# Kernel optimization log

Measured on AMD Instinct MI355X. Metric: run time of the kernel, lower is better.

## Reference

```python
import jax, jax.numpy as jnp
import numpy as np

TOP_K = 8


def setup_inputs() -> dict:
    key = jax.random.key(0)
    k1, k2 = jax.random.split(key)
    B, S, D, E = 4, 4096, 2048, 64
    x = jax.random.normal(k1, (B, S, D), dtype=jnp.float32)
    # nn.Linear(d_model, n_experts): weight [E, D], bias [E]
    W = jax.random.normal(k2, (E, D), dtype=jnp.float32) * (1.0 / np.sqrt(D))
    b = jnp.zeros((E,), dtype=jnp.float32)
    return {"x": x, "W": W, "b": b}


def reference(x, W, b):
    # logits: [B, S, E] = x @ W^T + b
    logits = jnp.einsum("bsd,ed->bse", x, W) + b
    scores = jax.nn.sigmoid(logits)                      # [B, S, E]
    B, S, E = scores.shape
    flat = scores.reshape(B * S, E)                      # tokens x experts
    top_w, top_idx = jax.lax.top_k(flat, TOP_K)          # [B*S, k]
    return top_w.reshape(B, S, TOP_K), top_idx.reshape(B, S, TOP_K)
```

## Files before the change

kernel.cpp:

```cpp
#include <hip/hip_runtime.h>
#include <math.h>

#define TOKENS 16384
#define DMODEL 2048
#define NEXP   64
#define TOPK   8
#define BM     32
#define BK     64
#define NCHUNK (DMODEL / BK)
#define ROWU   72
#define WTILEU (NEXP * ROWU)
#define WT3PAD 14336

typedef unsigned short u16;
typedef float f32x4 __attribute__((ext_vector_type(4)));
typedef short s16x8 __attribute__((ext_vector_type(8)));

__device__ __forceinline__ u16 f2bf(float f, float& back) {
    unsigned u = __float_as_uint(f);
    unsigned r = u + 0x7fffu + ((u >> 16) & 1u);
    back = __uint_as_float(r & 0xffff0000u);
    return (u16)(r >> 16);
}

__device__ __forceinline__ void gload_lds16(const void* g, void* l) {
    __builtin_amdgcn_global_load_lds(
        (const __attribute__((address_space(1))) unsigned int*)g,
        (__attribute__((address_space(3))) unsigned int*)l, 16, 0, 0);
}

__global__ __launch_bounds__(256) void wconv(
    const float* __restrict__ W, u16* __restrict__ wimg)
{
    const int id = blockIdx.x * 256 + threadIdx.x;
    const int e = id >> 11;
    const int k = id & 2047;
    const float x = W[id];
    float f1, f2, fd;
    const u16 a = f2bf(x, f1);
    const float d1 = x - f1;
    const u16 b = f2bf(d1, f2);
    const float d2 = d1 - f2;
    const u16 c = f2bf(d2, fd);
    u16* base = wimg + (size_t)(k >> 6) * WT3PAD + e * ROWU + (k & 63);
    base[0]          = a;
    base[WTILEU]     = b;
    base[2 * WTILEU] = c;
}

__global__ __launch_bounds__(256) void router_fused(
    const float* __restrict__ x, const u16* __restrict__ wimg,
    const float* __restrict__ bias, float* __restrict__ out_w,
    float* __restrict__ out_i)
{
    __shared__ __align__(16) u16 xs[3][BM * ROWU];
    __shared__ __align__(16) u16 wsb[2][WT3PAD];
    __shared__ float lg[BM][NEXP + 4];

    const int tid  = threadIdx.x;
    const int lane = tid & 63;
    const int w    = tid >> 6;
    const int wr   = w >> 1;
    const int wc   = w & 1;
    const size_t tokBase = (size_t)blockIdx.x * BM;

    const int srow = tid >> 3;
    const int soct = tid & 7;
    const float* xp = x + (tokBase + srow) * DMODEL + soct * 8;

    const int arow  = wr * 16 + (lane & 15);
    const int kq    = (lane >> 4) * 8;
    const int brow0 = wc * 32 + (lane & 15);

    f32x4  acc[2][2];
    double accd[2][4];
#pragma unroll
    for (int i = 0; i < 2; ++i)
#pragma unroll
        for (int j = 0; j < 2; ++j)
            acc[i][j] = (f32x4){0.f, 0.f, 0.f, 0.f};
#pragma unroll
    for (int j = 0; j < 2; ++j)
#pragma unroll
        for (int r = 0; r < 4; ++r) accd[j][r] = 0.0;

    const char* wgbase = (const char*)wimg;
#define WCOPY(tt, buf)                                                        \
    {                                                                         \
        const char* gsrc_ = wgbase + (size_t)(tt) * (WT3PAD * 2) + w * 1024 + \
                            lane * 16;                                        \
        char* ldst_ = (char*)&wsb[buf][0] + w * 1024;                         \
        _Pragma("unroll") for (int r_ = 0; r_ < 7; ++r_)                      \
            gload_lds16(gsrc_ + r_ * 4096, ldst_ + r_ * 4096);                \
    }

    float4 xa = *(const float4*)(xp);
    float4 xb = *(const float4*)(xp + 4);
    WCOPY(0, 0);

    for (int t = 0; t < NCHUNK; ++t) {
        __syncthreads();
        {
            float xv[8] = {xa.x, xa.y, xa.z, xa.w, xb.x, xb.y, xb.z, xb.w};
            s16x8 va, vb, vc;
#pragma unroll
            for (int j = 0; j < 8; ++j) {
                float f1, f2, fd;
                const u16 a1 = f2bf(xv[j], f1);
                const float d1 = xv[j] - f1;
                const u16 a2 = f2bf(d1, f2);
                const float d2 = d1 - f2;
                const u16 a3 = f2bf(d2, fd);
                va[j] = (short)a1; vb[j] = (short)a2; vc[j] = (short)a3;
            }
            const int ub = srow * ROWU + soct * 8;
            *(s16x8*)&xs[0][ub] = va;
            *(s16x8*)&xs[1][ub] = vb;
            *(s16x8*)&xs[2][ub] = vc;
        }
        __syncthreads();
        if (t + 1 < NCHUNK) {
            xp += BK;
            xa = *(const float4*)(xp);
            xb = *(const float4*)(xp + 4);
            WCOPY(t + 1, (t + 1) & 1);
        }

        const u16* wb = &wsb[t & 1][0];
#pragma unroll
        for (int ks = 0; ks < 2; ++ks) {
            const int ko = ks * 32 + kq;
            const s16x8 a1 = *(const s16x8*)&xs[0][arow * ROWU + ko];
            const s16x8 a2 = *(const s16x8*)&xs[1][arow * ROWU + ko];
            const s16x8 a3 = *(const s16x8*)&xs[2][arow * ROWU + ko];
#pragma unroll
            for (int nt = 0; nt < 2; ++nt) {
                const int br = (brow0 + nt * 16) * ROWU + ko;
                const s16x8 b1 = *(const s16x8*)&wb[0 * WTILEU + br];
                const s16x8 b2 = *(const s16x8*)&wb[1 * WTILEU + br];
                const s16x8 b3 = *(const s16x8*)&wb[2 * WTILEU + br];
                f32x4 t0 = acc[ks][nt];
                t0 = __builtin_amdgcn_mfma_f32_16x16x32_bf16(a1, b1, t0, 0, 0, 0);
                t0 = __builtin_amdgcn_mfma_f32_16x16x32_bf16(a1, b2, t0, 0, 0, 0);
                t0 = __builtin_amdgcn_mfma_f32_16x16x32_bf16(a2, b1, t0, 0, 0, 0);
                t0 = __builtin_amdgcn_mfma_f32_16x16x32_bf16(a1, b3, t0, 0, 0, 0);
                t0 = __builtin_amdgcn_mfma_f32_16x16x32_bf16(a3, b1, t0, 0, 0, 0);
                t0 = __builtin_amdgcn_mfma_f32_16x16x32_bf16(a2, b2, t0, 0, 0, 0);
                acc[ks][nt] = t0;
            }
        }
#pragma unroll
        for (int nt = 0; nt < 2; ++nt)
#pragma unroll
            for (int r = 0; r < 4; ++r) {
                accd[nt][r] += (double)acc[0][nt][r] + (double)acc[1][nt][r];
                acc[0][nt][r] = 0.f;
                acc[1][nt][r] = 0.f;
            }
    }

#pragma unroll
    for (int nt = 0; nt < 2; ++nt)
#pragma unroll
        for (int r = 0; r < 4; ++r) {
            const int row = wr * 16 + (lane >> 4) * 4 + r;
            const int col = wc * 32 + nt * 16 + (lane & 15);
            lg[row][col] = (float)accd[nt][r];
        }
    __syncthreads();

    const float be = bias[lane];
#pragma unroll
    for (int i = 0; i < 8; ++i) {
        const int tl = w * 8 + i;
        float v = lg[tl][lane] + be;
        const int myi = lane;
        float bv = 0.0f; int bi = 0;
#pragma unroll
        for (int r = 0; r < TOPK; ++r) {
            float mv = v; int mi = myi;
#pragma unroll
            for (int off = 32; off > 0; off >>= 1) {
                const float ov = __shfl_xor(mv, off, 64);
                const int   oi = __shfl_xor(mi, off, 64);
                if (ov > mv || (ov == mv && oi < mi)) { mv = ov; mi = oi; }
            }
            if (lane == r) { bv = mv; bi = mi; }
            if (myi == mi) { v = -INFINITY; }
        }
        if (lane < TOPK) {
            const size_t tok = tokBase + tl;
            out_w[tok * TOPK + lane] = 1.0f / (1.0f + expf(-bv));
            out_i[tok * TOPK + lane] = (float)bi;
        }
    }
}

extern "C" void kernel_launch(void* const* d_in, const int* in_sizes, int n_in,
                              void* d_out, int out_size, void* d_ws, size_t ws_size,
                              hipStream_t stream) {
    const float* x    = (const float*)d_in[0];
    const float* W    = (const float*)d_in[1];
    const float* bias = (const float*)d_in[2];
    float* out_w = (float*)d_out;
    float* out_i = (float*)d_out + (size_t)TOKENS * TOPK;
    u16* wimg = (u16*)d_ws;

    wconv<<<dim3((NEXP * DMODEL) / 256), 256, 0, stream>>>(W, wimg);
    router_fused<<<dim3(TOKENS / BM), 256, 0, stream>>>(x, wimg, bias, out_w, out_i);
}
```

Before: 259.4 us.

## Load x fragments directly to registers and pre-swizzle W into MFMA fragment layout

Each thread now loads its own x fragment from global memory straight into registers and splits it into three bf16 parts there, so the x shared-memory staging and one barrier per chunk go away. The weight-prep kernel writes W already arranged in MFMA B-fragment order, so the main kernel reads conflict-free s16x8 values. The weight chunk now goes through registers with a manual double buffer instead of direct global-to-LDS loads. The cost is that each wave repeats the x split for its own tile, register pressure rises, and shared memory is reused for the logits, which lowers the LDS footprint.

```diff
diff --git a/kernel.cpp b/kernel.cpp
--- a/kernel.cpp
+++ b/kernel.cpp
@@ -8,9 +8,8 @@
 #define BM     32
 #define BK     64
 #define NCHUNK (DMODEL / BK)
-#define ROWU   72
-#define WTILEU (NEXP * ROWU)
-#define WT3PAD 14336
+#define WCHUNKB 24576
+#define WSHORTS 12288
 
 typedef unsigned short u16;
 typedef float f32x4 __attribute__((ext_vector_type(4)));
@@ -23,29 +22,38 @@
     return (u16)(r >> 16);
 }
 
-__device__ __forceinline__ void gload_lds16(const void* g, void* l) {
-    __builtin_amdgcn_global_load_lds(
-        (const __attribute__((address_space(1))) unsigned int*)g,
-        (__attribute__((address_space(3))) unsigned int*)l, 16, 0, 0);
-}
-
 __global__ __launch_bounds__(256) void wconv(
     const float* __restrict__ W, u16* __restrict__ wimg)
 {
-    const int id = blockIdx.x * 256 + threadIdx.x;
-    const int e = id >> 11;
-    const int k = id & 2047;
-    const float x = W[id];
-    float f1, f2, fd;
-    const u16 a = f2bf(x, f1);
-    const float d1 = x - f1;
-    const u16 b = f2bf(d1, f2);
-    const float d2 = d1 - f2;
-    const u16 c = f2bf(d2, fd);
-    u16* base = wimg + (size_t)(k >> 6) * WT3PAD + e * ROWU + (k & 63);
-    base[0]          = a;
-    base[WTILEU]     = b;
-    base[2 * WTILEU] = c;
+    const int id  = blockIdx.x * 256 + threadIdx.x;
+    const int e   = id >> 8;
+    const int ko8 = id & 255;
+    const int k0  = ko8 * 8;
+    const int c   = ko8 >> 3;
+    const int ks  = (ko8 >> 2) & 1;
+    const int hi  = ko8 & 3;
+    const int lane = hi * 16 + (e & 15);
+    const int eq   = e >> 4;
+
+    const float* src = W + (size_t)e * DMODEL + k0;
+    const float4 f0 = *(const float4*)(src);
+    const float4 f1 = *(const float4*)(src + 4);
+    const float xe[8] = {f0.x, f0.y, f0.z, f0.w, f1.x, f1.y, f1.z, f1.w};
+    s16x8 va, vb, vc;
+#pragma unroll
+    for (int j = 0; j < 8; ++j) {
+        float b1, b2, b3;
+        const u16 a1 = f2bf(xe[j], b1);
+        const float d1 = xe[j] - b1;
+        const u16 a2 = f2bf(d1, b2);
+        const float d2 = d1 - b2;
+        const u16 a3 = f2bf(d2, b3);
+        va[j] = (short)a1; vb[j] = (short)a2; vc[j] = (short)a3;
+    }
+    u16* base = wimg + (size_t)c * WSHORTS + lane * 8;
+    *(s16x8*)(base + ((0 * 2 + ks) * 4 + eq) * 512) = va;
+    *(s16x8*)(base + ((1 * 2 + ks) * 4 + eq) * 512) = vb;
+    *(s16x8*)(base + ((2 * 2 + ks) * 4 + eq) * 512) = vc;
 }
 
 __global__ __launch_bounds__(256) void router_fused(
@@ -53,9 +61,7 @@
     const float* __restrict__ bias, float* __restrict__ out_w,
     float* __restrict__ out_i)
 {
-    __shared__ __align__(16) u16 xs[3][BM * ROWU];
-    __shared__ __align__(16) u16 wsb[2][WT3PAD];
-    __shared__ float lg[BM][NEXP + 4];
+    __shared__ __align__(16) u16 ws[2][WSHORTS];
 
     const int tid  = threadIdx.x;
     const int lane = tid & 63;
@@ -64,88 +70,87 @@
     const int wc   = w & 1;
     const size_t tokBase = (size_t)blockIdx.x * BM;
 
-    const int srow = tid >> 3;
-    const int soct = tid & 7;
-    const float* xp = x + (tokBase + srow) * DMODEL + soct * 8;
-
-    const int arow  = wr * 16 + (lane & 15);
-    const int kq    = (lane >> 4) * 8;
-    const int brow0 = wc * 32 + (lane & 15);
+    const int arow = wr * 16 + (lane & 15);
+    const float* xrow = x + (tokBase + arow) * (size_t)DMODEL + (lane >> 4) * 8;
+
+    const int eq0 = wc * 2;
 
     f32x4  acc[2][2];
     double accd[2][4];
 #pragma unroll
     for (int i = 0; i < 2; ++i)
 #pragma unroll
-        for (int j = 0; j < 2; ++j)
-            acc[i][j] = (f32x4){0.f, 0.f, 0.f, 0.f};
+        for (int j = 0; j < 2; ++j) acc[i][j] = (f32x4){0.f, 0.f, 0.f, 0.f};
 #pragma unroll
     for (int j = 0; j < 2; ++j)
 #pragma unroll
         for (int r = 0; r < 4; ++r) accd[j][r] = 0.0;
 
-    const char* wgbase = (const char*)wimg;
-#define WCOPY(tt, buf)                                                        \
-    {                                                                         \
-        const char* gsrc_ = wgbase + (size_t)(tt) * (WT3PAD * 2) + w * 1024 + \
-                            lane * 16;                                        \
-        char* ldst_ = (char*)&wsb[buf][0] + w * 1024;                         \
-        _Pragma("unroll") for (int r_ = 0; r_ < 7; ++r_)                      \
-            gload_lds16(gsrc_ + r_ * 4096, ldst_ + r_ * 4096);                \
-    }
-
-    float4 xa = *(const float4*)(xp);
-    float4 xb = *(const float4*)(xp + 4);
-    WCOPY(0, 0);
+    const char* wg = (const char*)wimg + tid * 16;
+    float4 wst[6];
+#pragma unroll
+    for (int r = 0; r < 6; ++r) wst[r] = *(const float4*)(wg + r * 4096);
+    float4 xv[4];
+#pragma unroll
+    for (int ks = 0; ks < 2; ++ks) {
+        xv[ks * 2 + 0] = *(const float4*)(xrow + ks * 32);
+        xv[ks * 2 + 1] = *(const float4*)(xrow + ks * 32 + 4);
+    }
+    {
+        char* wl = (char*)&ws[0][0] + tid * 16;
+#pragma unroll
+        for (int r = 0; r < 6; ++r) *(float4*)(wl + r * 4096) = wst[r];
+    }
+    __syncthreads();
 
     for (int t = 0; t < NCHUNK; ++t) {
-        __syncthreads();
-        {
-            float xv[8] = {xa.x, xa.y, xa.z, xa.w, xb.x, xb.y, xb.z, xb.w};
-            s16x8 va, vb, vc;
+        s16x8 af[3][2];
+#pragma unroll
+        for (int ks = 0; ks < 2; ++ks) {
+            const float xe[8] = {xv[ks * 2].x,     xv[ks * 2].y,
+                                 xv[ks * 2].z,     xv[ks * 2].w,
+                                 xv[ks * 2 + 1].x, xv[ks * 2 + 1].y,
+                                 xv[ks * 2 + 1].z, xv[ks * 2 + 1].w};
 #pragma unroll
             for (int j = 0; j < 8; ++j) {
-                float f1, f2, fd;
-                const u16 a1 = f2bf(xv[j], f1);
-                const float d1 = xv[j] - f1;
-                const u16 a2 = f2bf(d1, f2);
-                const float d2 = d1 - f2;
-                const u16 a3 = f2bf(d2, fd);
-                va[j] = (short)a1; vb[j] = (short)a2; vc[j] = (short)a3;
-            }
-            const int ub = srow * ROWU + soct * 8;
-            *(s16x8*)&xs[0][ub] = va;
-            *(s16x8*)&xs[1][ub] = vb;
-            *(s16x8*)&xs[2][ub] = vc;
-        }
-        __syncthreads();
+                float b1, b2, b3;
+                const u16 a1 = f2bf(xe[j], b1);
+                const float d1 = xe[j] - b1;
+                const u16 a2 = f2bf(d1, b2);
+                const float d2 = d1 - b2;
+                const u16 a3 = f2bf(d2, b3);
+                af[0][ks][j] = (short)a1;
+                af[1][ks][j] = (short)a2;
+                af[2][ks][j] = (short)a3;
+            }
+        }
         if (t + 1 < NCHUNK) {
-            xp += BK;
-            xa = *(const float4*)(xp);
-            xb = *(const float4*)(xp + 4);
-            WCOPY(t + 1, (t + 1) & 1);
-        }
-
-        const u16* wb = &wsb[t & 1][0];
+            const float* xp = xrow + (size_t)(t + 1) * BK;
+#pragma unroll
+            for (int ks = 0; ks < 2; ++ks) {
+                xv[ks * 2 + 0] = *(const float4*)(xp + ks * 32);
+                xv[ks * 2 + 1] = *(const float4*)(xp + ks * 32 + 4);
+            }
+            const char* wgp = wg + (size_t)(t + 1) * WCHUNKB;
+#pragma unroll
+            for (int r = 0; r < 6; ++r) wst[r] = *(const float4*)(wgp + r * 4096);
+        }
+        const u16* wb = &ws[t & 1][0];
 #pragma unroll
         for (int ks = 0; ks < 2; ++ks) {
-            const int ko = ks * 32 + kq;
-            const s16x8 a1 = *(const s16x8*)&xs[0][arow * ROWU + ko];
-            const s16x8 a2 = *(const s16x8*)&xs[1][arow * ROWU + ko];
-            const s16x8 a3 = *(const s16x8*)&xs[2][arow * ROWU + ko];
 #pragma unroll
             for (int nt = 0; nt < 2; ++nt) {
-                const int br = (brow0 + nt * 16) * ROWU + ko;
-                const s16x8 b1 = *(const s16x8*)&wb[0 * WTILEU + br];
-                const s16x8 b2 = *(const s16x8*)&wb[1 * WTILEU + br];
-                const s16x8 b3 = *(const s16x8*)&wb[2 * WTILEU + br];
+                const u16* bp = wb + (size_t)(eq0 + nt) * 512 + lane * 8;
+                const s16x8 b1 = *(const s16x8*)(bp + ((0 * 2 + ks) * 4) * 512);
+                const s16x8 b2 = *(const s16x8*)(bp + ((1 * 2 + ks) * 4) * 512);
+                const s16x8 b3 = *(const s16x8*)(bp + ((2 * 2 + ks) * 4) * 512);
                 f32x4 t0 = acc[ks][nt];
-                t0 = __builtin_amdgcn_mfma_f32_16x16x32_bf16(a1, b1, t0, 0, 0, 0);
-                t0 = __builtin_amdgcn_mfma_f32_16x16x32_bf16(a1, b2, t0, 0, 0, 0);
-                t0 = __builtin_amdgcn_mfma_f32_16x16x32_bf16(a2, b1, t0, 0, 0, 0);
-                t0 = __builtin_amdgcn_mfma_f32_16x16x32_bf16(a1, b3, t0, 0, 0, 0);
-                t0 = __builtin_amdgcn_mfma_f32_16x16x32_bf16(a3, b1, t0, 0, 0, 0);
-                t0 = __builtin_amdgcn_mfma_f32_16x16x32_bf16(a2, b2, t0, 0, 0, 0);
+                t0 = __builtin_amdgcn_mfma_f32_16x16x32_bf16(af[0][ks], b1, t0, 0, 0, 0);
+                t0 = __builtin_amdgcn_mfma_f32_16x16x32_bf16(af[0][ks], b2, t0, 0, 0, 0);
+                t0 = __builtin_amdgcn_mfma_f32_16x16x32_bf16(af[1][ks], b1, t0, 0, 0, 0);
+                t0 = __builtin_amdgcn_mfma_f32_16x16x32_bf16(af[0][ks], b3, t0, 0, 0, 0);
+                t0 = __builtin_amdgcn_mfma_f32_16x16x32_bf16(af[2][ks], b1, t0, 0, 0, 0);
+                t0 = __builtin_amdgcn_mfma_f32_16x16x32_bf16(af[1][ks], b2, t0, 0, 0, 0);
                 acc[ks][nt] = t0;
             }
         }
@@ -157,15 +162,22 @@
                 acc[0][nt][r] = 0.f;
                 acc[1][nt][r] = 0.f;
             }
-    }
-
+        if (t + 1 < NCHUNK) {
+            char* wl = (char*)&ws[(t + 1) & 1][0] + tid * 16;
+#pragma unroll
+            for (int r = 0; r < 6; ++r) *(float4*)(wl + r * 4096) = wst[r];
+        }
+        __syncthreads();
+    }
+
+    float* lg = (float*)&ws[0][0];
 #pragma unroll
     for (int nt = 0; nt < 2; ++nt)
 #pragma unroll
         for (int r = 0; r < 4; ++r) {
             const int row = wr * 16 + (lane >> 4) * 4 + r;
             const int col = wc * 32 + nt * 16 + (lane & 15);
-            lg[row][col] = (float)accd[nt][r];
+            lg[row * 68 + col] = (float)accd[nt][r];
         }
     __syncthreads();
 
@@ -173,7 +185,7 @@
 #pragma unroll
     for (int i = 0; i < 8; ++i) {
         const int tl = w * 8 + i;
-        float v = lg[tl][lane] + be;
+        float v = lg[tl * 68 + lane] + be;
         const int myi = lane;
         float bv = 0.0f; int bi = 0;
 #pragma unroll
@@ -206,6 +218,6 @@
     float* out_i = (float*)d_out + (size_t)TOKENS * TOPK;
     u16* wimg = (u16*)d_ws;
 
-    wconv<<<dim3((NEXP * DMODEL) / 256), 256, 0, stream>>>(W, wimg);
+    wconv<<<dim3((NEXP * DMODEL / 8) / 256), 256, 0, stream>>>(W, wimg);
     router_fused<<<dim3(TOKENS / BM), 256, 0, stream>>>(x, wimg, bias, out_w, out_i);
 }
```

Result: faster. 249.6 us (-3.8%).
